# Performance work log

Hardware: AMD Instinct MI355X
Metric: run time of the kernel (lower is better)

Reference implementation:

```python
import jax, jax.numpy as jnp
import numpy as np

B, C, H, W = 4, 256, 64, 64
C8 = C // 8


def setup_inputs() -> dict:
    key = jax.random.key(0)
    ks = jax.random.split(key, 9)
    s_in = 1.0 / np.sqrt(C)
    return {
        "x": jax.random.normal(ks[0], (B, C, H, W), dtype=jnp.float32),
        "Wq": jax.random.normal(ks[1], (C8, C), dtype=jnp.float32) * s_in,
        "bq": jax.random.normal(ks[2], (C8,), dtype=jnp.float32) * 0.01,
        "Wk": jax.random.normal(ks[3], (C8, C), dtype=jnp.float32) * s_in,
        "bk": jax.random.normal(ks[4], (C8,), dtype=jnp.float32) * 0.01,
        "Wv": jax.random.normal(ks[5], (C, C), dtype=jnp.float32) * s_in,
        "bv": jax.random.normal(ks[6], (C,), dtype=jnp.float32) * 0.01,
        "Wo": jax.random.normal(ks[7], (C, C), dtype=jnp.float32) * s_in,
        "bo": jax.random.normal(ks[8], (C,), dtype=jnp.float32) * 0.01,
    }


def reference(x, Wq, bq, Wk, bk, Wv, bv, Wo, bo):
    b, c, h, w = x.shape
    n = h * w
    xf = x.reshape(b, c, n)                                   # (B, C, N)
    # 1x1 convs are channel GEMMs
    q = jnp.einsum('bcn,dc->bnd', xf, Wq) + bq                # (B, N, C8)
    k = jnp.einsum('bcn,dc->bdn', xf, Wk) + bk[:, None]       # (B, C8, N)
    v = jnp.einsum('bcn,dc->bdn', xf, Wv) + bv[:, None]       # (B, C, N)
    energy = jnp.einsum('bnd,bdm->bnm', q, k)                 # (B, N, N)
    attn = jax.nn.softmax(energy, axis=-1)
    # out[b,c,i] = sum_j v[b,c,j] * attn[b,i,j]
    out = jnp.einsum('bcj,bij->bci', v, attn)                 # (B, C, N)
    out = out.reshape(b, c, h, w) + x                         # residual
    out = jnp.einsum('bchw,dc->bdhw', out, Wo) + bo[None, :, None, None]
    return out
```

## Files before the change

### kernel.cpp

```cpp
#include <hip/hip_runtime.h>

#define DEV __device__ __forceinline__

constexpr int B_  = 4;
constexpr int C_  = 256;
constexpr int C8_ = 32;
constexpr int N_  = 4096;
constexpr float LOG2E = 1.4426950408889634f;

using u16 = unsigned short;
using u32 = unsigned int;

typedef __attribute__((ext_vector_type(8))) short bf16x8;
typedef __attribute__((ext_vector_type(4))) float f32x4;

DEV float bf2f(u16 u) { return __uint_as_float(((u32)u) << 16); }
DEV u16   f2bf(float f) {
  u32 i = __float_as_uint(f);
  i += 0x7fffu + ((i >> 16) & 1u);
  return (u16)(i >> 16);
}

DEV void lds_barrier() {
  asm volatile("s_waitcnt lgkmcnt(0)\n\ts_barrier" ::: "memory");
}

__global__ __launch_bounds__(256) void wsplit(
    const float* __restrict__ Wq, const float* __restrict__ Wk,
    const float* __restrict__ Wv, const float* __restrict__ Wo,
    u16* __restrict__ WqH, u16* __restrict__ WqL,
    u16* __restrict__ WkH, u16* __restrict__ WkL,
    u16* __restrict__ WvH,
    u16* __restrict__ WoH, u16* __restrict__ WoL)
{
  int i = blockIdx.x * 256 + threadIdx.x;
  if (i < 8192) {
    float v = Wq[i] * LOG2E;
    u16 h = f2bf(v); WqH[i] = h; WqL[i] = f2bf(v - bf2f(h));
  } else if (i < 16384) {
    int off = i - 8192;
    float v = Wk[off];
    u16 h = f2bf(v); WkH[off] = h; WkL[off] = f2bf(v - bf2f(h));
  } else if (i < 81920) {
    int off = i - 16384;
    WvH[off] = f2bf(Wv[off]);
  } else {
    int off = i - 81920;
    float v = Wo[off];
    u16 h = f2bf(v); WoH[off] = h; WoL[off] = f2bf(v - bf2f(h));
  }
}

__global__ __launch_bounds__(256) void xprep(
    const float* __restrict__ x, u16* __restrict__ xTh, u16* __restrict__ xTl)
{
  __shared__ float tf[64][65];
  const int tid = threadIdx.x;
  const int b = blockIdx.z, c0 = blockIdx.y * 64, n0 = blockIdx.x * 64;
  const int nl = tid & 63, cb = tid >> 6;

  #pragma unroll
  for (int cc = 0; cc < 16; ++cc) {
    int cl = cb * 16 + cc;
    tf[nl][cl] = x[((size_t)b * C_ + c0 + cl) * N_ + n0 + nl];
  }
  __syncthreads();

  #pragma unroll
  for (int it = 0; it < 2; ++it) {
    int idx = tid + it * 256;
    int n = idx >> 3, q = idx & 7;
    u32 ph[4], pl[4];
    #pragma unroll
    for (int j = 0; j < 4; ++j) {
      float v0 = tf[n][q * 8 + 2 * j], v1 = tf[n][q * 8 + 2 * j + 1];
      u16 h0 = f2bf(v0), h1 = f2bf(v1);
      ph[j] = (u32)h0 | ((u32)h1 << 16);
      pl[j] = (u32)f2bf(v0 - bf2f(h0)) | ((u32)f2bf(v1 - bf2f(h1)) << 16);
    }
    size_t off = ((size_t)b * N_ + n0 + n) * C_ + c0 + q * 8;
    *(uint4*)&xTh[off] = make_uint4(ph[0], ph[1], ph[2], ph[3]);
    *(uint4*)&xTl[off] = make_uint4(pl[0], pl[1], pl[2], pl[3]);
  }
}

__global__ __launch_bounds__(256) void qkv_mfma(
    const u16* __restrict__ xTh, const u16* __restrict__ xTl,
    const u16* __restrict__ WqH, const u16* __restrict__ WqL,
    const u16* __restrict__ WkH, const u16* __restrict__ WkL,
    const u16* __restrict__ WvH,
    const float* __restrict__ bq, const float* __restrict__ bk,
    const float* __restrict__ bv,
    u16* __restrict__ qt, u16* __restrict__ kt, u16* __restrict__ vb)
{
  __shared__ __align__(16) u16 xsh[32][270];
  __shared__ __align__(16) u16 xsl[32][270];

  const int tid = threadIdx.x;
  const int lane = tid & 63, w = tid >> 6, m = lane & 15, quad = lane >> 4;
  const int b = blockIdx.y, n0 = blockIdx.x * 32;

  #pragma unroll
  for (int it = 0; it < 4; ++it) {
    int chunk = tid + it * 256;
    int row = chunk >> 5, col = (chunk & 31) * 8;
    size_t g = ((size_t)b * N_ + n0 + row) * C_ + col;
    *(uint4*)&xsh[row][col] = *(const uint4*)(xTh + g);
    *(uint4*)&xsl[row][col] = *(const uint4*)(xTl + g);
  }
  __syncthreads();

  const u16* qkH = (w < 2) ? (WqH + (size_t)(w * 16 + m) * C_)
                           : (WkH + (size_t)((w - 2) * 16 + m) * C_);
  const u16* qkL = (w < 2) ? (WqL + (size_t)(w * 16 + m) * C_)
                           : (WkL + (size_t)((w - 2) * 16 + m) * C_);

  f32x4 ov[4][2], oq[2];
  #pragma unroll
  for (int dt = 0; dt < 4; ++dt)
    #pragma unroll
    for (int nt = 0; nt < 2; ++nt) ov[dt][nt] = (f32x4){0.f, 0.f, 0.f, 0.f};
  #pragma unroll
  for (int nt = 0; nt < 2; ++nt) oq[nt] = (f32x4){0.f, 0.f, 0.f, 0.f};

  for (int K = 0; K < 8; ++K) {
    const int ko = K * 32 + quad * 8;
    bf16x8 xh[2], xl[2];
    #pragma unroll
    for (int nt = 0; nt < 2; ++nt) {
      xh[nt] = *(const bf16x8*)&xsh[nt * 16 + m][ko];
      xl[nt] = *(const bf16x8*)&xsl[nt * 16 + m][ko];
    }
    #pragma unroll
    for (int dt = 0; dt < 4; ++dt) {
      bf16x8 whi = *(const bf16x8*)(WvH + (size_t)(64 * w + dt * 16 + m) * C_ + ko);
      #pragma unroll
      for (int nt = 0; nt < 2; ++nt)
        ov[dt][nt] = __builtin_amdgcn_mfma_f32_16x16x32_bf16(whi, xh[nt], ov[dt][nt], 0, 0, 0);
    }
    {
      bf16x8 bhi = *(const bf16x8*)(qkH + ko);
      bf16x8 blo = *(const bf16x8*)(qkL + ko);
      #pragma unroll
      for (int nt = 0; nt < 2; ++nt) {
        oq[nt] = __builtin_amdgcn_mfma_f32_16x16x32_bf16(xh[nt], bhi, oq[nt], 0, 0, 0);
        oq[nt] = __builtin_amdgcn_mfma_f32_16x16x32_bf16(xl[nt], bhi, oq[nt], 0, 0, 0);
        oq[nt] = __builtin_amdgcn_mfma_f32_16x16x32_bf16(xh[nt], blo, oq[nt], 0, 0, 0);
      }
    }
  }

  #pragma unroll
  for (int dt = 0; dt < 4; ++dt)
    #pragma unroll
    for (int r = 0; r < 4; ++r) {
      int oc = 64 * w + dt * 16 + quad * 4 + r;
      float bias = bv[oc];
      #pragma unroll
      for (int nt = 0; nt < 2; ++nt)
        vb[((size_t)b * C_ + oc) * N_ + n0 + nt * 16 + m] = f2bf(ov[dt][nt][r] + bias);
    }
  {
    u16* qk_out = (w < 2) ? qt : kt;
    int dbase = (w & 1) * 16;
    float bias = (w < 2) ? bq[dbase + m] * LOG2E : bk[dbase + m];
    #pragma unroll
    for (int nt = 0; nt < 2; ++nt)
      #pragma unroll
      for (int r = 0; r < 4; ++r)
        qk_out[((size_t)b * N_ + n0 + nt * 16 + quad * 4 + r) * C8_ + dbase + m] =
            f2bf(oq[nt][r] + bias);
  }
}

__global__ __launch_bounds__(256) void attn_mfma(
    const u16* __restrict__ qt, const u16* __restrict__ kt,
    const u16* __restrict__ vb,
    float* __restrict__ Opart, float* __restrict__ ml)
{
  __shared__ __align__(16) u16  ps[2][64][136];
  __shared__ __align__(16) float als[2][64];

  const int tid = threadIdx.x, lane = tid & 63, w = tid >> 6;
  const int m = lane & 15, quad = lane >> 4;

  const int lid = blockIdx.x + gridDim.x * (blockIdx.y + gridDim.y * blockIdx.z);
  const int grp = lid & 7, ksl = grp & 1, b = grp >> 1;
  const int i0 = (lid >> 3) * 64;

  const bf16x8 qfrag =
      *(const bf16x8*)(qt + ((size_t)b * N_ + i0 + w * 16 + m) * C8_ + quad * 8);
  const u16* kbase = kt + (size_t)b * N_ * C8_;
  const u16* vrow  = vb + ((size_t)b * C_ + w * 64 + m) * N_;

  f32x4 o[4][4];
  #pragma unroll
  for (int t = 0; t < 4; ++t)
    #pragma unroll
    for (int ct = 0; ct < 4; ++ct) o[t][ct] = (f32x4){0.f, 0.f, 0.f, 0.f};
  float m_r = -1e30f, l_r = 0.f;

  const int jbeg = ksl * 2048, jend = jbeg + 2048;
  int buf = 0;

  for (int j0 = jbeg; j0 < jend; j0 += 128, buf ^= 1) {
    bf16x8 kA[8];
    #pragma unroll
    for (int t = 0; t < 8; ++t)
      kA[t] = *(const bf16x8*)(kbase + (size_t)(j0 + t * 16 + m) * C8_ + quad * 8);
    bf16x8 vB[4][4];
    #pragma unroll
    for (int ct = 0; ct < 4; ++ct)
      #pragma unroll
      for (int kk = 0; kk < 4; ++kk)
        vB[ct][kk] = *(const bf16x8*)(vrow + (size_t)ct * 16 * N_ + j0 + kk * 32 + quad * 8);

    f32x4 s[8];
    #pragma unroll
    for (int t = 0; t < 8; ++t)
      s[t] = __builtin_amdgcn_mfma_f32_16x16x32_bf16(
          kA[t], qfrag, (f32x4){0.f, 0.f, 0.f, 0.f}, 0, 0, 0);

    float mx = -1e30f;
    #pragma unroll
    for (int t = 0; t < 8; ++t)
      #pragma unroll
      for (int r = 0; r < 4; ++r) mx = fmaxf(mx, s[t][r]);
    mx = fmaxf(mx, __shfl_xor(mx, 16));
    mx = fmaxf(mx, __shfl_xor(mx, 32));
    float mn = fmaxf(m_r, mx);
    float al = exp2f(m_r - mn);
    m_r = mn;
    float p[8][4], sm = 0.f;
    #pragma unroll
    for (int t = 0; t < 8; ++t)
      #pragma unroll
      for (int r = 0; r < 4; ++r) {
        p[t][r] = exp2f(s[t][r] - mn);
        sm += p[t][r];
      }
    sm += __shfl_xor(sm, 16);
    sm += __shfl_xor(sm, 32);
    l_r = l_r * al + sm;

    #pragma unroll
    for (int t = 0; t < 8; ++t) {
      u32 lo = (u32)f2bf(p[t][0]) | ((u32)f2bf(p[t][1]) << 16);
      u32 hi = (u32)f2bf(p[t][2]) | ((u32)f2bf(p[t][3]) << 16);
      *(uint2*)&ps[buf][w * 16 + m][t * 16 + quad * 4] = make_uint2(lo, hi);
    }
    if (quad == 0) als[buf][w * 16 + m] = al;

    lds_barrier();

    #pragma unroll
    for (int t = 0; t < 4; ++t) {
      float4 alv = *(const float4*)&als[buf][t * 16 + quad * 4];
      #pragma unroll
      for (int ct = 0; ct < 4; ++ct) {
        o[t][ct][0] *= alv.x; o[t][ct][1] *= alv.y;
        o[t][ct][2] *= alv.z; o[t][ct][3] *= alv.w;
      }
    }

    #pragma unroll
    for (int t = 0; t < 4; ++t) {
      #pragma unroll
      for (int kk = 0; kk < 4; ++kk) {
        bf16x8 pf = *(const bf16x8*)&ps[buf][t * 16 + m][kk * 32 + quad * 8];
        #pragma unroll
        for (int ct = 0; ct < 4; ++ct)
          o[t][ct] = __builtin_amdgcn_mfma_f32_16x16x32_bf16(pf, vB[ct][kk], o[t][ct], 0, 0, 0);
      }
    }
  }

  float* Ob = Opart + (size_t)ksl * B_ * N_ * C_ + ((size_t)b * N_ + i0) * C_ + w * 64;
  #pragma unroll
  for (int t = 0; t < 4; ++t)
    #pragma unroll
    for (int ct = 0; ct < 4; ++ct)
      #pragma unroll
      for (int r = 0; r < 4; ++r)
        Ob[(size_t)(t * 16 + quad * 4 + r) * C_ + ct * 16 + m] = o[t][ct][r];

  if (quad == 0) {
    size_t mli = ((size_t)ksl * B_ + b) * N_ + i0 + w * 16 + m;
    ml[mli] = m_r;
    ml[(size_t)2 * B_ * N_ + mli] = l_r;
  }
}

__global__ __launch_bounds__(256) void combine_h(
    const float* __restrict__ Opart, const float* __restrict__ ml,
    const u16* __restrict__ xTh, u16* __restrict__ hB)
{
  const int tid = threadIdx.x;
  const int b = blockIdx.y, n0 = blockIdx.x * 64;
  constexpr size_t BN = (size_t)B_ * N_;
  const int lanec = tid & 15;

  #pragma unroll
  for (int pass = 0; pass < 4; ++pass) {
    int row = (tid >> 4) + pass * 16;
    size_t nrow = (size_t)b * N_ + n0 + row;
    float m0 = ml[nrow], m1 = ml[BN + nrow];
    float l0 = ml[2 * BN + nrow], l1 = ml[3 * BN + nrow];
    float M = fmaxf(m0, m1);
    float a0 = exp2f(m0 - M), a1 = exp2f(m1 - M);
    float inv = 1.f / (l0 * a0 + l1 * a1);
    float w0 = a0 * inv, w1 = a1 * inv;

    const float* O0 = Opart + nrow * C_;
    const float* O1 = O0 + BN * C_;
    #pragma unroll
    for (int i = 0; i < 4; ++i) {
      int c = lanec * 4 + i * 64;
      float4 a  = *(const float4*)(O0 + c);
      float4 c2 = *(const float4*)(O1 + c);
      uint2 xv = *(const uint2*)(xTh + nrow * C_ + c);
      float h0 = a.x * w0 + c2.x * w1 + bf2f((u16)(xv.x & 0xffff));
      float h1 = a.y * w0 + c2.y * w1 + bf2f((u16)(xv.x >> 16));
      float h2 = a.z * w0 + c2.z * w1 + bf2f((u16)(xv.y & 0xffff));
      float h3 = a.w * w0 + c2.w * w1 + bf2f((u16)(xv.y >> 16));
      u32 lo = (u32)f2bf(h0) | ((u32)f2bf(h1) << 16);
      u32 hi = (u32)f2bf(h2) | ((u32)f2bf(h3) << 16);
      *(uint2*)&hB[nrow * C_ + c] = make_uint2(lo, hi);
    }
  }
}

__global__ __launch_bounds__(256) void out_mfma(
    const u16* __restrict__ hB,
    const u16* __restrict__ WoH, const u16* __restrict__ WoL,
    const float* __restrict__ bo, float* __restrict__ out)
{
  __shared__ __align__(16) u16 hs[32][270];

  const int tid = threadIdx.x;
  const int lane = tid & 63, w = tid >> 6, m = lane & 15, quad = lane >> 4;
  const int b = blockIdx.y, n0 = blockIdx.x * 32;

  #pragma unroll
  for (int it = 0; it < 4; ++it) {
    int chunk = tid + it * 256;
    int row = chunk >> 5, col = (chunk & 31) * 8;
    *(uint4*)&hs[row][col] = *(const uint4*)(hB + ((size_t)b * N_ + n0 + row) * C_ + col);
  }
  __syncthreads();

  f32x4 o[4][2];
  #pragma unroll
  for (int dt = 0; dt < 4; ++dt)
    #pragma unroll
    for (int nt = 0; nt < 2; ++nt) o[dt][nt] = (f32x4){0.f, 0.f, 0.f, 0.f};

  for (int K = 0; K < 8; ++K) {
    const int ko = K * 32 + quad * 8;
    bf16x8 hf[2];
    #pragma unroll
    for (int nt = 0; nt < 2; ++nt) hf[nt] = *(const bf16x8*)&hs[nt * 16 + m][ko];
    #pragma unroll
    for (int dt = 0; dt < 4; ++dt) {
      bf16x8 whi = *(const bf16x8*)(WoH + (size_t)(64 * w + dt * 16 + m) * C_ + ko);
      bf16x8 wlo = *(const bf16x8*)(WoL + (size_t)(64 * w + dt * 16 + m) * C_ + ko);
      #pragma unroll
      for (int nt = 0; nt < 2; ++nt) {
        o[dt][nt] = __builtin_amdgcn_mfma_f32_16x16x32_bf16(whi, hf[nt], o[dt][nt], 0, 0, 0);
        o[dt][nt] = __builtin_amdgcn_mfma_f32_16x16x32_bf16(wlo, hf[nt], o[dt][nt], 0, 0, 0);
      }
    }
  }

  #pragma unroll
  for (int dt = 0; dt < 4; ++dt)
    #pragma unroll
    for (int r = 0; r < 4; ++r) {
      int d = 64 * w + dt * 16 + quad * 4 + r;
      float bias = bo[d];
      #pragma unroll
      for (int nt = 0; nt < 2; ++nt)
        out[((size_t)b * C_ + d) * N_ + n0 + nt * 16 + m] = o[dt][nt][r] + bias;
    }
}

extern "C" void kernel_launch(void* const* d_in, const int* in_sizes, int n_in,
                              void* d_out, int out_size, void* d_ws, size_t ws_size,
                              hipStream_t stream)
{
  const float* x  = (const float*)d_in[0];
  const float* Wq = (const float*)d_in[1];
  const float* bq = (const float*)d_in[2];
  const float* Wk = (const float*)d_in[3];
  const float* bk = (const float*)d_in[4];
  const float* Wv = (const float*)d_in[5];
  const float* bv = (const float*)d_in[6];
  const float* Wo = (const float*)d_in[7];
  const float* bo = (const float*)d_in[8];

  u16* p = (u16*)d_ws;
  u16* qt  = p;  p += (size_t)B_ * N_ * C8_;
  u16* kt  = p;  p += (size_t)B_ * N_ * C8_;
  u16* vb  = p;  p += (size_t)B_ * C_ * N_;
  u16* xTh = p;  p += (size_t)B_ * N_ * C_;
  u16* xTl = p;  p += (size_t)B_ * N_ * C_;
  u16* hB  = p;  p += (size_t)B_ * N_ * C_;
  u16* WqH = p;  p += 8192;
  u16* WqL = p;  p += 8192;
  u16* WkH = p;  p += 8192;
  u16* WkL = p;  p += 8192;
  u16* WvH = p;  p += 65536;
  u16* WoH = p;  p += 65536;
  u16* WoL = p;  p += 65536;
  float* Opart = (float*)p;
  float* ml = Opart + (size_t)2 * B_ * N_ * C_;

  float* out = (float*)d_out;

  wsplit<<<576, 256, 0, stream>>>(Wq, Wk, Wv, Wo,
      WqH, WqL, WkH, WkL, WvH, WoH, WoL);
  xprep<<<dim3(N_ / 64, C_ / 64, B_), 256, 0, stream>>>(x, xTh, xTl);
  qkv_mfma<<<dim3(N_ / 32, B_), 256, 0, stream>>>(
      xTh, xTl, WqH, WqL, WkH, WkL, WvH, bq, bk, bv, qt, kt, vb);
  attn_mfma<<<dim3(N_ / 64, 2, B_), 256, 0, stream>>>(qt, kt, vb, Opart, ml);
  combine_h<<<dim3(N_ / 64, B_), 256, 0, stream>>>(Opart, ml, xTh, hB);
  out_mfma<<<dim3(N_ / 32, B_), 256, 0, stream>>>(hB, WoH, WoL, bo, out);
}
```

Baseline: 216.7 us.

## Split attention keys four ways, store normalized bf16 partials, fuse combine into output GEMM

Measured after the change: 212.5 us. No clear change (-1.9%).

```diff
diff --git a/kernel.cpp b/kernel.cpp
--- a/kernel.cpp
+++ b/kernel.cpp
@@ -19,6 +19,9 @@
   u32 i = __float_as_uint(f);
   i += 0x7fffu + ((i >> 16) & 1u);
   return (u16)(i >> 16);
+}
+DEV u32 pack_rtz(float a, float b) {
+  return __builtin_amdgcn_perm(__float_as_uint(b), __float_as_uint(a), 0x07060302);
 }
 
 DEV void lds_barrier() {
@@ -176,17 +179,18 @@
 __global__ __launch_bounds__(256) void attn_mfma(
     const u16* __restrict__ qt, const u16* __restrict__ kt,
     const u16* __restrict__ vb,
-    float* __restrict__ Opart, float* __restrict__ ml)
+    u16* __restrict__ Onorm, float* __restrict__ ml)
 {
   __shared__ __align__(16) u16  ps[2][64][136];
   __shared__ __align__(16) float als[2][64];
+  __shared__ float lfin[64];
 
   const int tid = threadIdx.x, lane = tid & 63, w = tid >> 6;
   const int m = lane & 15, quad = lane >> 4;
 
   const int lid = blockIdx.x + gridDim.x * (blockIdx.y + gridDim.y * blockIdx.z);
-  const int grp = lid & 7, ksl = grp & 1, b = grp >> 1;
-  const int i0 = (lid >> 3) * 64;
+  const int grp = lid & 15, ksl = grp & 3, b = grp >> 2;
+  const int i0 = (lid >> 4) * 64;
 
   const bf16x8 qfrag =
       *(const bf16x8*)(qt + ((size_t)b * N_ + i0 + w * 16 + m) * C8_ + quad * 8);
@@ -200,7 +204,7 @@
     for (int ct = 0; ct < 4; ++ct) o[t][ct] = (f32x4){0.f, 0.f, 0.f, 0.f};
   float m_r = -1e30f, l_r = 0.f;
 
-  const int jbeg = ksl * 2048, jend = jbeg + 2048;
+  const int jbeg = ksl * 1024, jend = jbeg + 1024;
   int buf = 0;
 
   for (int j0 = jbeg; j0 < jend; j0 += 128, buf ^= 1) {
@@ -244,11 +248,9 @@
     l_r = l_r * al + sm;
 
     #pragma unroll
-    for (int t = 0; t < 8; ++t) {
-      u32 lo = (u32)f2bf(p[t][0]) | ((u32)f2bf(p[t][1]) << 16);
-      u32 hi = (u32)f2bf(p[t][2]) | ((u32)f2bf(p[t][3]) << 16);
-      *(uint2*)&ps[buf][w * 16 + m][t * 16 + quad * 4] = make_uint2(lo, hi);
-    }
+    for (int t = 0; t < 8; ++t)
+      *(uint2*)&ps[buf][w * 16 + m][t * 16 + quad * 4] =
+          make_uint2(pack_rtz(p[t][0], p[t][1]), pack_rtz(p[t][2], p[t][3]));
     if (quad == 0) als[buf][w * 16 + m] = al;
 
     lds_barrier();
@@ -275,63 +277,31 @@
     }
   }
 
-  float* Ob = Opart + (size_t)ksl * B_ * N_ * C_ + ((size_t)b * N_ + i0) * C_ + w * 64;
-  #pragma unroll
-  for (int t = 0; t < 4; ++t)
+  if (quad == 0) lfin[w * 16 + m] = 1.f / l_r;
+  lds_barrier();
+
+  u16* Ob = Onorm + (((size_t)ksl * B_ + b) * N_ + i0) * C_ + w * 64;
+  #pragma unroll
+  for (int t = 0; t < 4; ++t) {
+    float4 lv = *(const float4*)&lfin[t * 16 + quad * 4];
+    float linv[4] = {lv.x, lv.y, lv.z, lv.w};
     #pragma unroll
     for (int ct = 0; ct < 4; ++ct)
       #pragma unroll
       for (int r = 0; r < 4; ++r)
-        Ob[(size_t)(t * 16 + quad * 4 + r) * C_ + ct * 16 + m] = o[t][ct][r];
+        Ob[(size_t)(t * 16 + quad * 4 + r) * C_ + ct * 16 + m] = f2bf(o[t][ct][r] * linv[r]);
+  }
 
   if (quad == 0) {
     size_t mli = ((size_t)ksl * B_ + b) * N_ + i0 + w * 16 + m;
     ml[mli] = m_r;
-    ml[(size_t)2 * B_ * N_ + mli] = l_r;
-  }
-}
-
-__global__ __launch_bounds__(256) void combine_h(
-    const float* __restrict__ Opart, const float* __restrict__ ml,
-    const u16* __restrict__ xTh, u16* __restrict__ hB)
-{
-  const int tid = threadIdx.x;
-  const int b = blockIdx.y, n0 = blockIdx.x * 64;
-  constexpr size_t BN = (size_t)B_ * N_;
-  const int lanec = tid & 15;
-
-  #pragma unroll
-  for (int pass = 0; pass < 4; ++pass) {
-    int row = (tid >> 4) + pass * 16;
-    size_t nrow = (size_t)b * N_ + n0 + row;
-    float m0 = ml[nrow], m1 = ml[BN + nrow];
-    float l0 = ml[2 * BN + nrow], l1 = ml[3 * BN + nrow];
-    float M = fmaxf(m0, m1);
-    float a0 = exp2f(m0 - M), a1 = exp2f(m1 - M);
-    float inv = 1.f / (l0 * a0 + l1 * a1);
-    float w0 = a0 * inv, w1 = a1 * inv;
-
-    const float* O0 = Opart + nrow * C_;
-    const float* O1 = O0 + BN * C_;
-    #pragma unroll
-    for (int i = 0; i < 4; ++i) {
-      int c = lanec * 4 + i * 64;
-      float4 a  = *(const float4*)(O0 + c);
-      float4 c2 = *(const float4*)(O1 + c);
-      uint2 xv = *(const uint2*)(xTh + nrow * C_ + c);
-      float h0 = a.x * w0 + c2.x * w1 + bf2f((u16)(xv.x & 0xffff));
-      float h1 = a.y * w0 + c2.y * w1 + bf2f((u16)(xv.x >> 16));
-      float h2 = a.z * w0 + c2.z * w1 + bf2f((u16)(xv.y & 0xffff));
-      float h3 = a.w * w0 + c2.w * w1 + bf2f((u16)(xv.y >> 16));
-      u32 lo = (u32)f2bf(h0) | ((u32)f2bf(h1) << 16);
-      u32 hi = (u32)f2bf(h2) | ((u32)f2bf(h3) << 16);
-      *(uint2*)&hB[nrow * C_ + c] = make_uint2(lo, hi);
-    }
+    ml[(size_t)4 * B_ * N_ + mli] = l_r;
   }
 }
 
 __global__ __launch_bounds__(256) void out_mfma(
-    const u16* __restrict__ hB,
+    const u16* __restrict__ Onorm, const float* __restrict__ ml,
+    const u16* __restrict__ xTh,
     const u16* __restrict__ WoH, const u16* __restrict__ WoL,
     const float* __restrict__ bo, float* __restrict__ out)
 {
@@ -340,12 +310,49 @@
   const int tid = threadIdx.x;
   const int lane = tid & 63, w = tid >> 6, m = lane & 15, quad = lane >> 4;
   const int b = blockIdx.y, n0 = blockIdx.x * 32;
+  constexpr size_t BN = (size_t)B_ * N_;
 
   #pragma unroll
   for (int it = 0; it < 4; ++it) {
     int chunk = tid + it * 256;
     int row = chunk >> 5, col = (chunk & 31) * 8;
-    *(uint4*)&hs[row][col] = *(const uint4*)(hB + ((size_t)b * N_ + n0 + row) * C_ + col);
+    size_t nrow = (size_t)b * N_ + n0 + row;
+
+    float mm0 = ml[nrow], mm1 = ml[BN + nrow], mm2 = ml[2 * BN + nrow], mm3 = ml[3 * BN + nrow];
+    float M = fmaxf(fmaxf(mm0, mm1), fmaxf(mm2, mm3));
+    float ws[4];
+    ws[0] = ml[4 * BN + nrow] * exp2f(mm0 - M);
+    ws[1] = ml[5 * BN + nrow] * exp2f(mm1 - M);
+    ws[2] = ml[6 * BN + nrow] * exp2f(mm2 - M);
+    ws[3] = ml[7 * BN + nrow] * exp2f(mm3 - M);
+    float inv = 1.f / (ws[0] + ws[1] + ws[2] + ws[3]);
+    #pragma unroll
+    for (int s = 0; s < 4; ++s) ws[s] *= inv;
+
+    uint4 xv = *(const uint4*)(xTh + nrow * C_ + col);
+    u32 xq[4] = {xv.x, xv.y, xv.z, xv.w};
+    float acc[8];
+    #pragma unroll
+    for (int j = 0; j < 4; ++j) {
+      acc[2 * j]     = bf2f((u16)(xq[j] & 0xffff));
+      acc[2 * j + 1] = bf2f((u16)(xq[j] >> 16));
+    }
+    #pragma unroll
+    for (int s = 0; s < 4; ++s) {
+      uint4 ovv = *(const uint4*)(Onorm + (s * BN + nrow) * C_ + col);
+      u32 oq[4] = {ovv.x, ovv.y, ovv.z, ovv.w};
+      #pragma unroll
+      for (int j = 0; j < 4; ++j) {
+        acc[2 * j]     += ws[s] * bf2f((u16)(oq[j] & 0xffff));
+        acc[2 * j + 1] += ws[s] * bf2f((u16)(oq[j] >> 16));
+      }
+    }
+    uint4 pk;
+    pk.x = (u32)f2bf(acc[0]) | ((u32)f2bf(acc[1]) << 16);
+    pk.y = (u32)f2bf(acc[2]) | ((u32)f2bf(acc[3]) << 16);
+    pk.z = (u32)f2bf(acc[4]) | ((u32)f2bf(acc[5]) << 16);
+    pk.w = (u32)f2bf(acc[6]) | ((u32)f2bf(acc[7]) << 16);
+    *(uint4*)&hs[row][col] = pk;
   }
   __syncthreads();
 
@@ -403,8 +410,6 @@
   u16* kt  = p;  p += (size_t)B_ * N_ * C8_;
   u16* vb  = p;  p += (size_t)B_ * C_ * N_;
   u16* xTh = p;  p += (size_t)B_ * N_ * C_;
-  u16* xTl = p;  p += (size_t)B_ * N_ * C_;
-  u16* hB  = p;  p += (size_t)B_ * N_ * C_;
   u16* WqH = p;  p += 8192;
   u16* WqL = p;  p += 8192;
   u16* WkH = p;  p += 8192;
@@ -412,8 +417,9 @@
   u16* WvH = p;  p += 65536;
   u16* WoH = p;  p += 65536;
   u16* WoL = p;  p += 65536;
-  float* Opart = (float*)p;
-  float* ml = Opart + (size_t)2 * B_ * N_ * C_;
+  float* ml = (float*)p;  p += (size_t)16 * B_ * N_;
+  u16* xTl   = p;
+  u16* Onorm = p;
 
   float* out = (float*)d_out;
 
@@ -422,7 +428,6 @@
   xprep<<<dim3(N_ / 64, C_ / 64, B_), 256, 0, stream>>>(x, xTh, xTl);
   qkv_mfma<<<dim3(N_ / 32, B_), 256, 0, stream>>>(
       xTh, xTl, WqH, WqL, WkH, WkL, WvH, bq, bk, bv, qt, kt, vb);
-  attn_mfma<<<dim3(N_ / 64, 2, B_), 256, 0, stream>>>(qt, kt, vb, Opart, ml);
-  combine_h<<<dim3(N_ / 64, B_), 256, 0, stream>>>(Opart, ml, xTh, hB);
-  out_mfma<<<dim3(N_ / 32, B_), 256, 0, stream>>>(hB, WoH, WoL, bo, out);
-}
+  attn_mfma<<<dim3(N_ / 64, 4, B_), 256, 0, stream>>>(qt, kt, vb, Onorm, ml);
+  out_mfma<<<dim3(N_ / 32, B_), 256, 0, stream>>>(Onorm, ml, xTh, WoH, WoL, bo, out);
+}
```
